# Kernel optimization log

Hardware: AMD Instinct MI355X
Metric: run time of the kernel (lower is better)

The kernel has to match this reference:

```python
import jax, jax.numpy as jnp
import numpy as np

IN_DIM = 128
OUT_DIM = 128
NUM_HEADS = 4
HEAD_DIM = OUT_DIM // NUM_HEADS
TEMP = 0.2
NEG_SLOPE = 0.2


def _xavier(key, shape, gain=1.414):
    fan_in, fan_out = shape[-2], shape[-1]
    limit = gain * np.sqrt(6.0 / (fan_in + fan_out))
    return jax.random.uniform(key, shape, jnp.float32, -limit, limit)


def setup_inputs() -> dict:
    key = jax.random.key(0)
    k_h, k_W, k_a, k_mw, k_mb = jax.random.split(key, 5)
    B, N = 4, 2048
    h = jax.random.normal(k_h, (B, N, IN_DIM), jnp.float32)
    W = _xavier(k_W, (NUM_HEADS, IN_DIM, HEAD_DIM))
    a = _xavier(k_a, (NUM_HEADS, 2 * HEAD_DIM, 1))
    merge_w = _xavier(k_mw, (OUT_DIM, OUT_DIM))  # nn.Linear weight [out, in]
    merge_b = jnp.zeros((OUT_DIM,), jnp.float32)
    return {"h": h, "W": W, "a": a, "merge_w": merge_w, "merge_b": merge_b}


def reference(h, W, a, merge_w, merge_b):
    B, N, _ = h.shape
    # Wh: [B, H, N, head_dim]
    Wh = jnp.einsum('bni,hio->bhno', h, W)
    a_sq = a[..., 0]                                  # [H, 2*hd]
    a_src, a_dst = a_sq[:, :HEAD_DIM], a_sq[:, HEAD_DIM:]
    # additive score decomposition avoids the NxNx2hd concat blowup
    s_src = jnp.einsum('bhno,ho->bhn', Wh, a_src)     # contribution of node i (row)
    s_dst = jnp.einsum('bhno,ho->bhn', Wh, a_dst)     # contribution of node j (col)
    e = s_src[:, :, :, None] + s_dst[:, :, None, :]   # [B, H, N, N]
    e = jnp.where(e > 0, e, NEG_SLOPE * e)            # LeakyReLU(0.2)
    alpha = jax.nn.softmax(e / TEMP, axis=3)          # softmax over neighbors j
    h_prime_heads = jnp.einsum('bhnm,bhmo->bhno', alpha, Wh)
    h_concat = h_prime_heads.transpose(0, 2, 1, 3).reshape(B, N, OUT_DIM)
    h_prime = h_concat @ merge_w.T + merge_b
    return h_prime, alpha.mean(axis=1)
```

## Files before the change

kernel.cpp:

```cpp
#include <hip/hip_runtime.h>
#include <stddef.h>

#define NN 2048
#define DIN 128
#define HD 32

typedef __attribute__((ext_vector_type(8))) short short8;
typedef __attribute__((ext_vector_type(4))) float f32x4;

constexpr float SLOPE = 0.2f;
constexpr float LC = 7.2134752044448170f;

__device__ __forceinline__ unsigned int pack_rne(float a, float b){
    unsigned int xa = __float_as_uint(a), xb = __float_as_uint(b);
    unsigned int ra = (xa + 0x7fffu + ((xa >> 16) & 1u)) >> 16;
    unsigned int rb = (xb + 0x7fffu + ((xb >> 16) & 1u)) >> 16;
    return ra | (rb << 16);
}

__global__ __launch_bounds__(256) void kWh(const float* __restrict__ hg,
                                           const float* __restrict__ Wg,
                                           float* __restrict__ Wh)
{
    __shared__ float Wl[DIN*HD];
    __shared__ float Hl[8][DIN+4];
    const int t = threadIdx.x;
    const int bh = blockIdx.x >> 5;
    const int tile = blockIdx.x & 31;
    const int b = bh >> 2, hh = bh & 3;
    for (int i = t; i < DIN*HD; i += 256) Wl[i] = Wg[hh*DIN*HD + i];
    const int o = t & 31, r = t >> 5;
    for (int it = 0; it < 8; ++it){
        const int nb = tile*64 + it*8;
        __syncthreads();
        {
            const float4 v = *(const float4*)&hg[((size_t)b*NN + nb + r)*DIN + o*4];
            *(float4*)&Hl[r][o*4] = v;
        }
        __syncthreads();
        float acc = 0.f;
        #pragma unroll 8
        for (int i = 0; i < DIN; ++i) acc = fmaf(Hl[r][i], Wl[i*HD+o], acc);
        Wh[((size_t)bh*NN + nb + r)*HD + o] = acc;
    }
}

__global__ __launch_bounds__(256) void kScore(const float* __restrict__ Wh,
                                              const float* __restrict__ ag,
                                              float* __restrict__ sSrc,
                                              float* __restrict__ sDst,
                                              float* __restrict__ maxPart)
{
    __shared__ float al[64];
    __shared__ float wred[4];
    const int t = threadIdx.x;
    const int bh = blockIdx.x >> 3, seg = blockIdx.x & 7;
    const int hh = bh & 3;
    if (t < 64) al[t] = ag[hh*64 + t];
    __syncthreads();
    const int n = seg*256 + t;
    const float4* wr = (const float4*)&Wh[((size_t)bh*NN + n)*HD];
    float ss = 0.f, sd = 0.f;
    #pragma unroll
    for (int q = 0; q < 8; ++q){
        float4 w = wr[q];
        ss += w.x*al[q*4+0] + w.y*al[q*4+1] + w.z*al[q*4+2] + w.w*al[q*4+3];
        sd += w.x*al[32+q*4+0] + w.y*al[32+q*4+1] + w.z*al[32+q*4+2] + w.w*al[32+q*4+3];
    }
    sSrc[bh*NN+n] = ss; sDst[bh*NN+n] = sd;
    float lmax = sd;
    #pragma unroll
    for (int off = 32; off > 0; off >>= 1) lmax = fmaxf(lmax, __shfl_down(lmax, off));
    if ((t & 63) == 0) wred[t >> 6] = lmax;
    __syncthreads();
    if (t == 0) maxPart[bh*8 + seg] = fmaxf(fmaxf(wred[0], wred[1]), fmaxf(wred[2], wred[3]));
}

__global__ __launch_bounds__(256) void kAttnM(const float* __restrict__ Wh,
                                              const float* __restrict__ sSrc,
                                              const float* __restrict__ sDst,
                                              const float* __restrict__ maxPart,
                                              float* __restrict__ invZ,
                                              unsigned short* __restrict__ hcb)
{
    __shared__ unsigned short WtT[32][136];
    __shared__ float sdl[128];
    const int t = threadIdx.x;
    const int wv = t >> 6, lane = t & 63;
    const int q = lane >> 4, c = lane & 15;
    const int bh = blockIdx.x >> 5;
    const int n0 = (blockIdx.x & 31)*64 + wv*16;
    const int b = bh >> 2, hh = bh & 3;
    float mx = maxPart[bh*8];
    #pragma unroll
    for (int i = 1; i < 8; ++i) mx = fmaxf(mx, maxPart[bh*8 + i]);
    const float ssrc = sSrc[bh*NN + n0 + c];
    const float q0 = ssrc + mx;
    const float R = fmaxf(q0, SLOPE*q0) * LC;
    const float a1 = ssrc*LC - R;
    const float a2 = SLOPE*LC*ssrc - R;
    f32x4 acc0 = {0.f,0.f,0.f,0.f}, acc1 = {0.f,0.f,0.f,0.f};
    float Zp = 0.f;
    const size_t whbase = (size_t)bh*NN*HD;
    for (int mt = 0; mt < 16; ++mt){
        const int mb = mt*128;
        __syncthreads();
        #pragma unroll
        for (int ii = 0; ii < 2; ++ii){
            const int idx = t + 256*ii;
            const int c4 = idx & 7, rp = idx >> 3;
            const float4 v0 = *(const float4*)&Wh[whbase + (size_t)(mb + 2*rp)*HD + c4*4];
            const float4 v1 = *(const float4*)&Wh[whbase + (size_t)(mb + 2*rp + 1)*HD + c4*4];
            const unsigned int* b0 = (const unsigned int*)&v0;
            const unsigned int* b1 = (const unsigned int*)&v1;
            #pragma unroll
            for (int k = 0; k < 4; ++k){
                unsigned int xa = b0[k], xb = b1[k];
                unsigned int pk = ((xa + 0x7fffu + ((xa>>16)&1u)) >> 16)
                                | (((xb + 0x7fffu + ((xb>>16)&1u)) >> 16) << 16);
                *(unsigned int*)&WtT[c4*4 + k][2*rp] = pk;
            }
        }
        if (t < 128) sdl[t] = LC * sDst[bh*NN + mb + t];
        __syncthreads();
        #pragma unroll
        for (int ks = 0; ks < 4; ++ks){
            const int m8 = ks*32 + q*8;
            float p[8];
            #pragma unroll
            for (int j = 0; j < 8; ++j){
                const float u = sdl[m8 + j];
                p[j] = exp2f(fmaxf(a1 + u, fmaf(SLOPE, u, a2)));
                Zp += p[j];
            }
            short8 aF;
            #pragma unroll
            for (int j = 0; j < 8; j += 2){
                ((unsigned int*)&aF)[j>>1] = (__float_as_uint(p[j]) >> 16)
                                           | (__float_as_uint(p[j+1]) & 0xffff0000u);
            }
            const short8 bF0 = *(const short8*)&WtT[c][m8];
            const short8 bF1 = *(const short8*)&WtT[16 + c][m8];
            acc0 = __builtin_amdgcn_mfma_f32_16x16x32_bf16(aF, bF0, acc0, 0, 0, 0);
            acc1 = __builtin_amdgcn_mfma_f32_16x16x32_bf16(aF, bF1, acc1, 0, 0, 0);
        }
    }
    Zp += __shfl_xor(Zp, 16);
    Zp += __shfl_xor(Zp, 32);
    const float iz = 1.0f / Zp;
    if (q == 0) invZ[bh*NN + n0 + c] = iz;
    #pragma unroll
    for (int reg = 0; reg < 4; ++reg){
        const int row = q*4 + reg;
        const float izr = __shfl(iz, row);
        const size_t base = ((size_t)b*NN + n0 + row)*128 + hh*32;
        hcb[base + c]      = (unsigned short)((pack_rne(acc0[reg]*izr, 0.f)) & 0xffffu);
        hcb[base + 16 + c] = (unsigned short)((pack_rne(acc1[reg]*izr, 0.f)) & 0xffffu);
    }
}

__global__ __launch_bounds__(256) void kAlpha(const float* __restrict__ sSrc,
                                              const float* __restrict__ sDst,
                                              const float* __restrict__ maxPart,
                                              const float* __restrict__ invZ,
                                              float* __restrict__ out1)
{
    __shared__ float sdl[4][NN];
    const int t = threadIdx.x;
    const int b = blockIdx.x >> 9;
    const int n0 = (blockIdx.x & 511) * 4;
    for (int i = t; i < 4*NN; i += 256)
        sdl[i >> 11][i & (NN-1)] = LC * sDst[(size_t)(b*4 + (i>>11))*NN + (i & (NN-1))];
    __syncthreads();
    float a1[4][4], a2[4][4], cf[4][4];
    #pragma unroll
    for (int hh = 0; hh < 4; ++hh){
        float mx = maxPart[(b*4+hh)*8];
        #pragma unroll
        for (int i = 1; i < 8; ++i) mx = fmaxf(mx, maxPart[(b*4+hh)*8 + i]);
        #pragma unroll
        for (int rr = 0; rr < 4; ++rr){
            const int bhn = (b*4+hh)*NN + n0 + rr;
            const float ss = sSrc[bhn];
            const float q0 = ss + mx;
            const float R = fmaxf(q0, SLOPE*q0)*LC;
            a1[rr][hh] = ss*LC - R;
            a2[rr][hh] = SLOPE*LC*ss - R;
            cf[rr][hh] = 0.25f * invZ[bhn];
        }
    }
    for (int mb = 0; mb < NN; mb += 256){
        const int m = mb + t;
        const float u0 = sdl[0][m], u1 = sdl[1][m], u2 = sdl[2][m], u3 = sdl[3][m];
        #pragma unroll
        for (int rr = 0; rr < 4; ++rr){
            float v;
            v  = cf[rr][0]*exp2f(fmaxf(a1[rr][0]+u0, fmaf(SLOPE, u0, a2[rr][0])));
            v += cf[rr][1]*exp2f(fmaxf(a1[rr][1]+u1, fmaf(SLOPE, u1, a2[rr][1])));
            v += cf[rr][2]*exp2f(fmaxf(a1[rr][2]+u2, fmaf(SLOPE, u2, a2[rr][2])));
            v += cf[rr][3]*exp2f(fmaxf(a1[rr][3]+u3, fmaf(SLOPE, u3, a2[rr][3])));
            out1[((size_t)b*NN + n0 + rr)*NN + m] = v;
        }
    }
}

__global__ __launch_bounds__(256) void kMergeM(const unsigned short* __restrict__ hcb,
                                               const float* __restrict__ mw,
                                               const float* __restrict__ mbv,
                                               float* __restrict__ out0)
{
    __shared__ unsigned short mwb[128][136];
    const int t = threadIdx.x;
    const int wv = t >> 6, lane = t & 63;
    const int q = lane >> 4, c = lane & 15;
    for (int i = t; i < 128*64; i += 256){
        const int j = i >> 6, k2 = i & 63;
        const float2 v = *(const float2*)&mw[j*128 + k2*2];
        *(unsigned int*)&mwb[j][k2*2] = pack_rne(v.x, v.y);
    }
    __syncthreads();
    const int row0 = blockIdx.x*64 + wv*16;
    f32x4 acc[8];
    #pragma unroll
    for (int ot = 0; ot < 8; ++ot) acc[ot] = (f32x4){0.f,0.f,0.f,0.f};
    #pragma unroll
    for (int ks = 0; ks < 4; ++ks){
        const short8 aF = *(const short8*)&hcb[((size_t)row0 + c)*128 + ks*32 + q*8];
        #pragma unroll
        for (int ot = 0; ot < 8; ++ot){
            const short8 bF = *(const short8*)&mwb[ot*16 + c][ks*32 + q*8];
            acc[ot] = __builtin_amdgcn_mfma_f32_16x16x32_bf16(aF, bF, acc[ot], 0, 0, 0);
        }
    }
    #pragma unroll
    for (int ot = 0; ot < 8; ++ot){
        const int col = ot*16 + c;
        const float bias = mbv[col];
        #pragma unroll
        for (int reg = 0; reg < 4; ++reg){
            const size_t row = (size_t)row0 + q*4 + reg;
            out0[row*128 + col] = acc[ot][reg] + bias;
        }
    }
}

extern "C" void kernel_launch(void* const* d_in, const int* in_sizes, int n_in,
                              void* d_out, int out_size, void* d_ws, size_t ws_size,
                              hipStream_t stream)
{
    const float* hg  = (const float*)d_in[0];
    const float* Wg  = (const float*)d_in[1];
    const float* ag  = (const float*)d_in[2];
    const float* mw  = (const float*)d_in[3];
    const float* mbv = (const float*)d_in[4];
    float* out0 = (float*)d_out;
    float* out1 = out0 + (size_t)4*NN*128;

    float* ws     = (float*)d_ws;
    float* Wh     = ws;
    float* sSrc   = Wh + 1048576;
    float* sDst   = sSrc + 32768;
    float* maxPart= sDst + 32768;
    float* invZ   = maxPart + 128;
    unsigned short* hcb = (unsigned short*)(invZ + 32768);

    hipLaunchKernelGGL(kWh,    dim3(512),  dim3(256), 0, stream, hg, Wg, Wh);
    hipLaunchKernelGGL(kScore, dim3(128),  dim3(256), 0, stream, Wh, ag, sSrc, sDst, maxPart);
    hipLaunchKernelGGL(kAttnM, dim3(512),  dim3(256), 0, stream, Wh, sSrc, sDst, maxPart, invZ, hcb);
    hipLaunchKernelGGL(kAlpha, dim3(2048), dim3(256), 0, stream, sSrc, sDst, maxPart, invZ, out1);
    hipLaunchKernelGGL(kMergeM,dim3(128),  dim3(256), 0, stream, hcb, mw, mbv, out0);
}
```

Baseline: 168.5 us.

## Pretranspose Wh to bf16 in score kernel; stream MFMA operands from global

The score kernel now also writes a transposed bf16 copy of Wh, laid out [bh][dim][node]. The attention kernel then loads B fragments for the MFMA directly from global memory with one-iteration register prefetch, and stages the whole sDst row in LDS once. This removes the per-tile fp32-to-bf16 conversion, the LDS transpose and the two barriers per tile in the hot loop. The cost is an extra workspace buffer, extra global writes in kScore, and uncoalesced-ish global reads that rely on cache.

```diff
diff --git a/kernel.cpp b/kernel.cpp
--- a/kernel.cpp
+++ b/kernel.cpp
@@ -16,6 +16,11 @@
     unsigned int ra = (xa + 0x7fffu + ((xa >> 16) & 1u)) >> 16;
     unsigned int rb = (xb + 0x7fffu + ((xb >> 16) & 1u)) >> 16;
     return ra | (rb << 16);
+}
+
+__device__ __forceinline__ unsigned short bf16_rne(float a){
+    unsigned int x = __float_as_uint(a);
+    return (unsigned short)((x + 0x7fffu + ((x >> 16) & 1u)) >> 16);
 }
 
 __global__ __launch_bounds__(256) void kWh(const float* __restrict__ hg,
@@ -49,10 +54,12 @@
                                               const float* __restrict__ ag,
                                               float* __restrict__ sSrc,
                                               float* __restrict__ sDst,
-                                              float* __restrict__ maxPart)
+                                              float* __restrict__ maxPart,
+                                              unsigned short* __restrict__ WhT)
 {
     __shared__ float al[64];
     __shared__ float wred[4];
+    __shared__ unsigned short Tl[32][264];
     const int t = threadIdx.x;
     const int bh = blockIdx.x >> 3, seg = blockIdx.x & 7;
     const int hh = bh & 3;
@@ -60,90 +67,92 @@
     __syncthreads();
     const int n = seg*256 + t;
     const float4* wr = (const float4*)&Wh[((size_t)bh*NN + n)*HD];
+    float4 w[8];
     float ss = 0.f, sd = 0.f;
     #pragma unroll
     for (int q = 0; q < 8; ++q){
-        float4 w = wr[q];
-        ss += w.x*al[q*4+0] + w.y*al[q*4+1] + w.z*al[q*4+2] + w.w*al[q*4+3];
-        sd += w.x*al[32+q*4+0] + w.y*al[32+q*4+1] + w.z*al[32+q*4+2] + w.w*al[32+q*4+3];
+        w[q] = wr[q];
+        ss += w[q].x*al[q*4+0] + w[q].y*al[q*4+1] + w[q].z*al[q*4+2] + w[q].w*al[q*4+3];
+        sd += w[q].x*al[32+q*4+0] + w[q].y*al[32+q*4+1] + w[q].z*al[32+q*4+2] + w[q].w*al[32+q*4+3];
     }
     sSrc[bh*NN+n] = ss; sDst[bh*NN+n] = sd;
+    #pragma unroll
+    for (int q = 0; q < 8; ++q){
+        const float* f = (const float*)&w[q];
+        #pragma unroll
+        for (int k2 = 0; k2 < 4; ++k2)
+            Tl[q*4+k2][t] = bf16_rne(f[k2]);
+    }
     float lmax = sd;
     #pragma unroll
     for (int off = 32; off > 0; off >>= 1) lmax = fmaxf(lmax, __shfl_down(lmax, off));
     if ((t & 63) == 0) wred[t >> 6] = lmax;
     __syncthreads();
+    {
+        const int o = t >> 3, ch = t & 7;
+        const size_t base = ((size_t)bh*32 + o)*NN + seg*256;
+        #pragma unroll
+        for (int k = 0; k < 4; ++k)
+            *(short8*)&WhT[base + k*64 + ch*8] = *(const short8*)&Tl[o][k*64 + ch*8];
+    }
     if (t == 0) maxPart[bh*8 + seg] = fmaxf(fmaxf(wred[0], wred[1]), fmaxf(wred[2], wred[3]));
 }
 
-__global__ __launch_bounds__(256) void kAttnM(const float* __restrict__ Wh,
+__global__ __launch_bounds__(256) void kAttnM(const unsigned short* __restrict__ WhT,
                                               const float* __restrict__ sSrc,
                                               const float* __restrict__ sDst,
                                               const float* __restrict__ maxPart,
                                               float* __restrict__ invZ,
                                               unsigned short* __restrict__ hcb)
 {
-    __shared__ unsigned short WtT[32][136];
-    __shared__ float sdl[128];
-    const int t = threadIdx.x;
-    const int wv = t >> 6, lane = t & 63;
+    __shared__ float sdl[NN];
+    const int t = threadIdx.x;
+    const int lane = t & 63;
+    const int wv = t >> 6;
     const int q = lane >> 4, c = lane & 15;
     const int bh = blockIdx.x >> 5;
     const int n0 = (blockIdx.x & 31)*64 + wv*16;
     const int b = bh >> 2, hh = bh & 3;
+    for (int i = t; i < NN; i += 256) sdl[i] = LC * sDst[bh*NN + i];
     float mx = maxPart[bh*8];
     #pragma unroll
     for (int i = 1; i < 8; ++i) mx = fmaxf(mx, maxPart[bh*8 + i]);
     const float ssrc = sSrc[bh*NN + n0 + c];
-    const float q0 = ssrc + mx;
-    const float R = fmaxf(q0, SLOPE*q0) * LC;
+    const float q0v = ssrc + mx;
+    const float R = fmaxf(q0v, SLOPE*q0v) * LC;
     const float a1 = ssrc*LC - R;
     const float a2 = SLOPE*LC*ssrc - R;
+    __syncthreads();
+    const unsigned short* wb0 = WhT + (size_t)bh*32*NN + (size_t)c*NN + q*8;
+    const unsigned short* wb1 = wb0 + (size_t)16*NN;
     f32x4 acc0 = {0.f,0.f,0.f,0.f}, acc1 = {0.f,0.f,0.f,0.f};
     float Zp = 0.f;
-    const size_t whbase = (size_t)bh*NN*HD;
-    for (int mt = 0; mt < 16; ++mt){
-        const int mb = mt*128;
-        __syncthreads();
-        #pragma unroll
-        for (int ii = 0; ii < 2; ++ii){
-            const int idx = t + 256*ii;
-            const int c4 = idx & 7, rp = idx >> 3;
-            const float4 v0 = *(const float4*)&Wh[whbase + (size_t)(mb + 2*rp)*HD + c4*4];
-            const float4 v1 = *(const float4*)&Wh[whbase + (size_t)(mb + 2*rp + 1)*HD + c4*4];
-            const unsigned int* b0 = (const unsigned int*)&v0;
-            const unsigned int* b1 = (const unsigned int*)&v1;
-            #pragma unroll
-            for (int k = 0; k < 4; ++k){
-                unsigned int xa = b0[k], xb = b1[k];
-                unsigned int pk = ((xa + 0x7fffu + ((xa>>16)&1u)) >> 16)
-                                | (((xb + 0x7fffu + ((xb>>16)&1u)) >> 16) << 16);
-                *(unsigned int*)&WtT[c4*4 + k][2*rp] = pk;
-            }
-        }
-        if (t < 128) sdl[t] = LC * sDst[bh*NN + mb + t];
-        __syncthreads();
-        #pragma unroll
-        for (int ks = 0; ks < 4; ++ks){
-            const int m8 = ks*32 + q*8;
-            float p[8];
-            #pragma unroll
-            for (int j = 0; j < 8; ++j){
-                const float u = sdl[m8 + j];
-                p[j] = exp2f(fmaxf(a1 + u, fmaf(SLOPE, u, a2)));
-                Zp += p[j];
-            }
-            short8 aF;
-            #pragma unroll
-            for (int j = 0; j < 8; j += 2){
-                ((unsigned int*)&aF)[j>>1] = (__float_as_uint(p[j]) >> 16)
-                                           | (__float_as_uint(p[j+1]) & 0xffff0000u);
-            }
-            const short8 bF0 = *(const short8*)&WtT[c][m8];
-            const short8 bF1 = *(const short8*)&WtT[16 + c][m8];
-            acc0 = __builtin_amdgcn_mfma_f32_16x16x32_bf16(aF, bF0, acc0, 0, 0, 0);
-            acc1 = __builtin_amdgcn_mfma_f32_16x16x32_bf16(aF, bF1, acc1, 0, 0, 0);
-        }
+    short8 bF0 = *(const short8*)&wb0[0];
+    short8 bF1 = *(const short8*)&wb1[0];
+    #pragma unroll 4
+    for (int it = 0; it < 64; ++it){
+        const int m8 = it*32 + q*8;
+        const int nx = ((it+1) & 63)*32;
+        const short8 nF0 = *(const short8*)&wb0[nx];
+        const short8 nF1 = *(const short8*)&wb1[nx];
+        const f32x4 u0 = *(const f32x4*)&sdl[m8];
+        const f32x4 u1 = *(const f32x4*)&sdl[m8+4];
+        float p[8];
+        #pragma unroll
+        for (int j = 0; j < 4; ++j){
+            p[j]   = exp2f(fmaxf(a1 + u0[j], fmaf(SLOPE, u0[j], a2)));
+            p[4+j] = exp2f(fmaxf(a1 + u1[j], fmaf(SLOPE, u1[j], a2)));
+        }
+        short8 aF;
+        #pragma unroll
+        for (int j = 0; j < 8; j += 2){
+            ((unsigned int*)&aF)[j>>1] = (__float_as_uint(p[j]) >> 16)
+                                       | (__float_as_uint(p[j+1]) & 0xffff0000u);
+            Zp += p[j] + p[j+1];
+        }
+        acc0 = __builtin_amdgcn_mfma_f32_16x16x32_bf16(aF, bF0, acc0, 0, 0, 0);
+        acc1 = __builtin_amdgcn_mfma_f32_16x16x32_bf16(aF, bF1, acc1, 0, 0, 0);
+        bF0 = nF0; bF1 = nF1;
     }
     Zp += __shfl_xor(Zp, 16);
     Zp += __shfl_xor(Zp, 32);
@@ -263,10 +272,11 @@
     float* maxPart= sDst + 32768;
     float* invZ   = maxPart + 128;
     unsigned short* hcb = (unsigned short*)(invZ + 32768);
+    unsigned short* WhT = hcb + 1048576;
 
     hipLaunchKernelGGL(kWh,    dim3(512),  dim3(256), 0, stream, hg, Wg, Wh);
-    hipLaunchKernelGGL(kScore, dim3(128),  dim3(256), 0, stream, Wh, ag, sSrc, sDst, maxPart);
-    hipLaunchKernelGGL(kAttnM, dim3(512),  dim3(256), 0, stream, Wh, sSrc, sDst, maxPart, invZ, hcb);
+    hipLaunchKernelGGL(kScore, dim3(128),  dim3(256), 0, stream, Wh, ag, sSrc, sDst, maxPart, WhT);
+    hipLaunchKernelGGL(kAttnM, dim3(512),  dim3(256), 0, stream, WhT, sSrc, sDst, maxPart, invZ, hcb);
     hipLaunchKernelGGL(kAlpha, dim3(2048), dim3(256), 0, stream, sSrc, sDst, maxPart, invZ, out1);
     hipLaunchKernelGGL(kMergeM,dim3(128),  dim3(256), 0, stream, hcb, mw, mbv, out0);
 }
```

New measurement: 165.8 us. Within noise of the previous version (-1.6%).
